# Performance work log

Hardware: AMD Instinct MI355X
Metric: run time of the kernel (lower is better)

The kernel has to match this reference:

```python
import jax, jax.numpy as jnp
import numpy as np

H = 2048          # uniform hidden size (num_in = layer_sizes[i] = num_out)
L = 8             # number of stacked LSTM cells = len(layer_sizes) + 1


def setup_inputs() -> dict:
    key = jax.random.key(0)
    ks = jax.random.split(key, 7)
    s = 1.0 / np.sqrt(H)  # torch default uniform(-1/sqrt(H), 1/sqrt(H)) scale
    return {
        "x": jax.random.normal(ks[0], (H,), dtype=jnp.float32),
        "w_ih": jax.random.normal(ks[1], (L, 4 * H, H), dtype=jnp.float32) * s,
        "w_hh": jax.random.normal(ks[2], (L, 4 * H, H), dtype=jnp.float32) * s,
        "b_ih": jax.random.normal(ks[3], (L, 4 * H), dtype=jnp.float32) * s,
        "b_hh": jax.random.normal(ks[4], (L, 4 * H), dtype=jnp.float32) * s,
        "h0": jax.random.uniform(ks[5], (L, 1, H), dtype=jnp.float32),
        "c0": jax.random.uniform(ks[6], (L, 1, H), dtype=jnp.float32),
    }


def _lstm_cell(x, h, c, w_ih, w_hh, b_ih, b_hh):
    # x, h, c: [1, H]; w_*: [4H, H]; PyTorch gate order: i, f, g, o
    gates = x @ w_ih.T + b_ih + h @ w_hh.T + b_hh  # [1, 4H]
    i, f, g, o = jnp.split(gates, 4, axis=-1)
    c_new = jax.nn.sigmoid(f) * c + jax.nn.sigmoid(i) * jnp.tanh(g)
    h_new = jax.nn.sigmoid(o) * jnp.tanh(c_new)
    return h_new, c_new


def reference(x, w_ih, w_hh, b_ih, b_hh, h0, c0):
    # seq_len = 1, batch = 1 (forward() does x.view(1, 1, -1))
    out = x.reshape(1, H)
    for l in range(L):
        h_new, _ = _lstm_cell(out, h0[l], c0[l], w_ih[l], w_hh[l], b_ih[l], b_hh[l])
        out = h_new
        if l < L - 1:  # tanh between layers, but not after the last cell
            out = jnp.tanh(out)
    return out.reshape(1, 1, H)
```

## Files before the change

kernel.cpp:

```cpp
#include <hip/hip_runtime.h>

#define HSZ 2048
#define NL  8

__global__ __launch_bounds__(256) void lstm_layer_kernel(
    const float* __restrict__ in,
    const float* __restrict__ w_ih,
    const float* __restrict__ w_hh,
    const float* __restrict__ b_ih,
    const float* __restrict__ b_hh,
    const float* __restrict__ h0,
    const float* __restrict__ c0,
    float* __restrict__ out,
    int apply_tanh)
{
    const int j    = blockIdx.x;
    const int wave = threadIdx.x >> 6;
    const int lane = threadIdx.x & 63;
    const int row  = wave * HSZ + j;

    const float4* __restrict__ wih4 = (const float4*)(w_ih + (size_t)row * HSZ);
    const float4* __restrict__ whh4 = (const float4*)(w_hh + (size_t)row * HSZ);
    const float4* __restrict__ in4  = (const float4*)in;
    const float4* __restrict__ h04  = (const float4*)h0;

    float acc = 0.f;
    #pragma unroll
    for (int it = 0; it < 8; ++it) {
        const int k = it * 64 + lane;
        float4 a  = wih4[k];
        float4 b  = whh4[k];
        float4 xv = in4[k];
        float4 hv = h04[k];
        acc += a.x * xv.x + a.y * xv.y + a.z * xv.z + a.w * xv.w;
        acc += b.x * hv.x + b.y * hv.y + b.z * hv.z + b.w * hv.w;
    }

    #pragma unroll
    for (int off = 32; off > 0; off >>= 1)
        acc += __shfl_down(acc, off, 64);

    __shared__ float gates[4];
    if (lane == 0) gates[wave] = acc + b_ih[row] + b_hh[row];
    __syncthreads();

    if (threadIdx.x == 0) {
        const float gi = gates[0];
        const float gf = gates[1];
        const float gg = gates[2];
        const float go = gates[3];
        const float si = 1.f / (1.f + __expf(-gi));
        const float sf = 1.f / (1.f + __expf(-gf));
        const float so = 1.f / (1.f + __expf(-go));
        const float tg = tanhf(gg);
        float c_new = sf * c0[j] + si * tg;
        float h     = so * tanhf(c_new);
        if (apply_tanh) h = tanhf(h);
        out[j] = h;
    }
}

extern "C" void kernel_launch(void* const* d_in, const int* in_sizes, int n_in,
                              void* d_out, int out_size, void* d_ws, size_t ws_size,
                              hipStream_t stream) {
    const float* x    = (const float*)d_in[0];
    const float* w_ih = (const float*)d_in[1];
    const float* w_hh = (const float*)d_in[2];
    const float* b_ih = (const float*)d_in[3];
    const float* b_hh = (const float*)d_in[4];
    const float* h0   = (const float*)d_in[5];
    const float* c0   = (const float*)d_in[6];
    float* out  = (float*)d_out;
    float* buf0 = (float*)d_ws;
    float* buf1 = buf0 + HSZ;

    const float* cur = x;
    for (int l = 0; l < NL; ++l) {
        float* o = (l == NL - 1) ? out : ((l & 1) ? buf1 : buf0);
        lstm_layer_kernel<<<HSZ, 256, 0, stream>>>(
            cur,
            w_ih + (size_t)l * 4 * HSZ * HSZ,
            w_hh + (size_t)l * 4 * HSZ * HSZ,
            b_ih + (size_t)l * 4 * HSZ,
            b_hh + (size_t)l * 4 * HSZ,
            h0 + (size_t)l * HSZ,
            c0 + (size_t)l * HSZ,
            o,
            (l < NL - 1) ? 1 : 0);
        cur = o;
    }
}
```

Baseline: 215.1 us.

## Fuse all LSTM layers into one persistent kernel with grid-wide atomic barrier

Replaces eight per-layer launches with a single persistent kernel of 1024 blocks, each handling two hidden units across all layers, synchronized between layers by an atomic counter barrier reset via memset. It removes launch overhead and inter-kernel gaps. It relies on all blocks being co-resident and adds spin-barrier latency plus a memset per call; the dot loops are also split into separate input and hidden passes.

After: 851.0 us. +295.7%, slower.

```diff
diff --git a/kernel.cpp b/kernel.cpp
--- a/kernel.cpp
+++ b/kernel.cpp
@@ -1,10 +1,24 @@
 #include <hip/hip_runtime.h>
 
-#define HSZ 2048
-#define NL  8
+#define HSZ  2048
+#define NL   8
+#define NBLK 1024
+#define NTHR 512
 
-__global__ __launch_bounds__(256) void lstm_layer_kernel(
-    const float* __restrict__ in,
+__device__ __forceinline__ void grid_sync(unsigned* cnt) {
+    __syncthreads();
+    if (threadIdx.x == 0) {
+        __threadfence();
+        __hip_atomic_fetch_add(cnt, 1u, __ATOMIC_RELEASE, __HIP_MEMORY_SCOPE_AGENT);
+        while (__hip_atomic_load(cnt, __ATOMIC_RELAXED, __HIP_MEMORY_SCOPE_AGENT) < NBLK)
+            __builtin_amdgcn_s_sleep(2);
+        (void)__hip_atomic_load(cnt, __ATOMIC_ACQUIRE, __HIP_MEMORY_SCOPE_AGENT);
+    }
+    __syncthreads();
+}
+
+__global__ __launch_bounds__(NTHR, 8) void lstm_fused_kernel(
+    const float* __restrict__ x,
     const float* __restrict__ w_ih,
     const float* __restrict__ w_hh,
     const float* __restrict__ b_ih,
@@ -12,51 +26,73 @@
     const float* __restrict__ h0,
     const float* __restrict__ c0,
     float* __restrict__ out,
-    int apply_tanh)
+    float* __restrict__ buf0,
+    float* __restrict__ buf1,
+    unsigned* __restrict__ bar_cnt)
 {
-    const int j    = blockIdx.x;
     const int wave = threadIdx.x >> 6;
     const int lane = threadIdx.x & 63;
-    const int row  = wave * HSZ + j;
+    const int gate = wave & 3;
+    const int j    = blockIdx.x + NBLK * (wave >> 2);
+    const int row  = gate * HSZ + j;
 
-    const float4* __restrict__ wih4 = (const float4*)(w_ih + (size_t)row * HSZ);
-    const float4* __restrict__ whh4 = (const float4*)(w_hh + (size_t)row * HSZ);
-    const float4* __restrict__ in4  = (const float4*)in;
-    const float4* __restrict__ h04  = (const float4*)h0;
+    __shared__ float gates[2][4];
 
-    float acc = 0.f;
-    #pragma unroll
-    for (int it = 0; it < 8; ++it) {
-        const int k = it * 64 + lane;
-        float4 a  = wih4[k];
-        float4 b  = whh4[k];
-        float4 xv = in4[k];
-        float4 hv = h04[k];
-        acc += a.x * xv.x + a.y * xv.y + a.z * xv.z + a.w * xv.w;
-        acc += b.x * hv.x + b.y * hv.y + b.z * hv.z + b.w * hv.w;
-    }
+    const float* cur = x;
+    for (int l = 0; l < NL; ++l) {
+        const float4* __restrict__ wih4 =
+            (const float4*)(w_ih + (size_t)l * 4 * HSZ * HSZ + (size_t)row * HSZ);
+        const float4* __restrict__ whh4 =
+            (const float4*)(w_hh + (size_t)l * 4 * HSZ * HSZ + (size_t)row * HSZ);
+        const float4* __restrict__ in4 = (const float4*)cur;
+        const float4* __restrict__ h4  = (const float4*)(h0 + (size_t)l * HSZ);
 
-    #pragma unroll
-    for (int off = 32; off > 0; off >>= 1)
-        acc += __shfl_down(acc, off, 64);
+        float acc = 0.f;
+        #pragma unroll
+        for (int it = 0; it < 8; ++it) {
+            const int k = it * 64 + lane;
+            float4 a  = wih4[k];
+            float4 xv = in4[k];
+            acc += a.x * xv.x + a.y * xv.y + a.z * xv.z + a.w * xv.w;
+        }
+        #pragma unroll
+        for (int it = 0; it < 8; ++it) {
+            const int k = it * 64 + lane;
+            float4 b  = whh4[k];
+            float4 hv = h4[k];
+            acc += b.x * hv.x + b.y * hv.y + b.z * hv.z + b.w * hv.w;
+        }
 
-    __shared__ float gates[4];
-    if (lane == 0) gates[wave] = acc + b_ih[row] + b_hh[row];
-    __syncthreads();
+        #pragma unroll
+        for (int off = 32; off > 0; off >>= 1)
+            acc += __shfl_down(acc, off, 64);
 
-    if (threadIdx.x == 0) {
-        const float gi = gates[0];
-        const float gf = gates[1];
-        const float gg = gates[2];
-        const float go = gates[3];
-        const float si = 1.f / (1.f + __expf(-gi));
-        const float sf = 1.f / (1.f + __expf(-gf));
-        const float so = 1.f / (1.f + __expf(-go));
-        const float tg = tanhf(gg);
-        float c_new = sf * c0[j] + si * tg;
-        float h     = so * tanhf(c_new);
-        if (apply_tanh) h = tanhf(h);
-        out[j] = h;
+        if (lane == 0)
+            gates[wave >> 2][gate] = acc + b_ih[(size_t)l * 4 * HSZ + row]
+                                         + b_hh[(size_t)l * 4 * HSZ + row];
+        __syncthreads();
+
+        float* obuf = (l == NL - 1) ? out : ((l & 1) ? buf1 : buf0);
+        if (threadIdx.x < 2) {
+            const int jj = blockIdx.x + (int)threadIdx.x * NBLK;
+            const float gi = gates[threadIdx.x][0];
+            const float gf = gates[threadIdx.x][1];
+            const float gg = gates[threadIdx.x][2];
+            const float go = gates[threadIdx.x][3];
+            const float si = 1.f / (1.f + __expf(-gi));
+            const float sf = 1.f / (1.f + __expf(-gf));
+            const float so = 1.f / (1.f + __expf(-go));
+            const float tg = tanhf(gg);
+            const float c_new = sf * c0[(size_t)l * HSZ + jj] + si * tg;
+            float h = so * tanhf(c_new);
+            if (l < NL - 1) h = tanhf(h);
+            obuf[jj] = h;
+        }
+
+        if (l < NL - 1) {
+            grid_sync(bar_cnt + l);
+            cur = obuf;
+        }
     }
 }
 
@@ -70,23 +106,13 @@
     const float* b_hh = (const float*)d_in[4];
     const float* h0   = (const float*)d_in[5];
     const float* c0   = (const float*)d_in[6];
-    float* out  = (float*)d_out;
-    float* buf0 = (float*)d_ws;
+    float* out = (float*)d_out;
+
+    unsigned* bar_cnt = (unsigned*)d_ws;
+    float* buf0 = (float*)((char*)d_ws + 256);
     float* buf1 = buf0 + HSZ;
 
-    const float* cur = x;
-    for (int l = 0; l < NL; ++l) {
-        float* o = (l == NL - 1) ? out : ((l & 1) ? buf1 : buf0);
-        lstm_layer_kernel<<<HSZ, 256, 0, stream>>>(
-            cur,
-            w_ih + (size_t)l * 4 * HSZ * HSZ,
-            w_hh + (size_t)l * 4 * HSZ * HSZ,
-            b_ih + (size_t)l * 4 * HSZ,
-            b_hh + (size_t)l * 4 * HSZ,
-            h0 + (size_t)l * HSZ,
-            c0 + (size_t)l * HSZ,
-            o,
-            (l < NL - 1) ? 1 : 0);
-        cur = o;
-    }
+    hipMemsetAsync(bar_cnt, 0, (NL - 1) * sizeof(unsigned), stream);
+    lstm_fused_kernel<<<NBLK, NTHR, 0, stream>>>(
+        x, w_ih, w_hh, b_ih, b_hh, h0, c0, out, buf0, buf1, bar_cnt);
 }
```

## Fuse all LSTM layers into one persistent kernel with grid-wide atomic barriers

Applied to the files above, without the earlier changes.

Replaces the eight per-layer launches with a single kernel of 2048 blocks that step through the layers, synchronising through hierarchical atomic counters (64 groups plus a master counter) held in workspace. Each block computes the recurrent w_hh·h0 dot product for the next layer before waiting on the barrier, which overlaps that weight streaming with the inter-layer dependency. Weights are read with nontemporal loads and the layer input is staged in LDS. This relies on all 2048 blocks being co-resident (8 per CU via launch bounds); otherwise the spin barrier deadlocks. It also adds a memset launch.

Measured after the change: 409.7 us. 90.5% more time.

```diff
diff --git a/kernel.cpp b/kernel.cpp
--- a/kernel.cpp
+++ b/kernel.cpp
@@ -1,10 +1,46 @@
 #include <hip/hip_runtime.h>
 
-#define HSZ 2048
-#define NL  8
+#define HSZ   2048
+#define NL    8
+#define NBLK  2048
+#define NTHR  256
+#define NGRP  64
+#define BPG   (NBLK/NGRP)
+#define BAR_U32 1040
 
-__global__ __launch_bounds__(256) void lstm_layer_kernel(
-    const float* __restrict__ in,
+typedef float f4 __attribute__((ext_vector_type(4)));
+
+__device__ __forceinline__ unsigned ld_rlx_u(const unsigned* p) {
+    return __hip_atomic_load(p, __ATOMIC_RELAXED, __HIP_MEMORY_SCOPE_AGENT);
+}
+__device__ __forceinline__ float ld_rlx_f(const float* p) {
+    return __hip_atomic_load(p, __ATOMIC_RELAXED, __HIP_MEMORY_SCOPE_AGENT);
+}
+__device__ __forceinline__ void st_rlx_f(float* p, float v) {
+    __hip_atomic_store(p, v, __ATOMIC_RELAXED, __HIP_MEMORY_SCOPE_AGENT);
+}
+__device__ __forceinline__ void arrive(unsigned* bar, int grp) {
+    unsigned o = __hip_atomic_fetch_add(&bar[grp * 16], 1u,
+                    __ATOMIC_RELAXED, __HIP_MEMORY_SCOPE_AGENT);
+    if (o == BPG - 1)
+        __hip_atomic_fetch_add(&bar[NGRP * 16], 1u,
+                    __ATOMIC_RELAXED, __HIP_MEMORY_SCOPE_AGENT);
+}
+
+__device__ __forceinline__ float dot8(const f4* __restrict__ w,
+                                      const f4* __restrict__ v, int lane) {
+    float acc = 0.f;
+    #pragma unroll
+    for (int i = 0; i < 8; ++i) {
+        f4 a = __builtin_nontemporal_load(&w[i * 64 + lane]);
+        f4 b = v[i * 64 + lane];
+        acc += a.x * b.x + a.y * b.y + a.z * b.z + a.w * b.w;
+    }
+    return acc;
+}
+
+__global__ __launch_bounds__(NTHR, 8) void lstm_fused(
+    const float* __restrict__ x,
     const float* __restrict__ w_ih,
     const float* __restrict__ w_hh,
     const float* __restrict__ b_ih,
@@ -12,51 +48,90 @@
     const float* __restrict__ h0,
     const float* __restrict__ c0,
     float* __restrict__ out,
-    int apply_tanh)
+    float* __restrict__ hA,
+    float* __restrict__ hB,
+    unsigned* __restrict__ bars)
 {
+    __shared__ float s_v[HSZ];
+    __shared__ float s_g[4];
+
+    const int tid  = threadIdx.x;
+    const int wave = tid >> 6;
+    const int lane = tid & 63;
     const int j    = blockIdx.x;
-    const int wave = threadIdx.x >> 6;
-    const int lane = threadIdx.x & 63;
     const int row  = wave * HSZ + j;
+    const int grp  = blockIdx.x & (NGRP - 1);
 
-    const float4* __restrict__ wih4 = (const float4*)(w_ih + (size_t)row * HSZ);
-    const float4* __restrict__ whh4 = (const float4*)(w_hh + (size_t)row * HSZ);
-    const float4* __restrict__ in4  = (const float4*)in;
-    const float4* __restrict__ h04  = (const float4*)h0;
-
-    float acc = 0.f;
-    #pragma unroll
-    for (int it = 0; it < 8; ++it) {
-        const int k = it * 64 + lane;
-        float4 a  = wih4[k];
-        float4 b  = whh4[k];
-        float4 xv = in4[k];
-        float4 hv = h04[k];
-        acc += a.x * xv.x + a.y * xv.y + a.z * xv.z + a.w * xv.w;
-        acc += b.x * hv.x + b.y * hv.y + b.z * hv.z + b.w * hv.w;
+    {
+        const f4* x4 = (const f4*)x;
+        f4* sv4 = (f4*)s_v;
+        sv4[tid]        = x4[tid];
+        sv4[tid + NTHR] = x4[tid + NTHR];
     }
-
-    #pragma unroll
-    for (int off = 32; off > 0; off >>= 1)
-        acc += __shfl_down(acc, off, 64);
-
-    __shared__ float gates[4];
-    if (lane == 0) gates[wave] = acc + b_ih[row] + b_hh[row];
     __syncthreads();
 
-    if (threadIdx.x == 0) {
-        const float gi = gates[0];
-        const float gf = gates[1];
-        const float gg = gates[2];
-        const float go = gates[3];
+    {
+        const float bs = b_ih[row] + b_hh[row];
+        const f4* wi4 = (const f4*)(w_ih + (size_t)row * HSZ);
+        const f4* wh4 = (const f4*)(w_hh + (size_t)row * HSZ);
+        float acc = dot8(wi4, (const f4*)s_v, lane)
+                  + dot8(wh4, (const f4*)h0, lane);
+        #pragma unroll
+        for (int off = 32; off; off >>= 1) acc += __shfl_down(acc, off, 64);
+        if (lane == 0) s_g[wave] = acc + bs;
+    }
+    __syncthreads();
+    if (tid == 0) {
+        const float gi = s_g[0], gf = s_g[1], gg = s_g[2], go = s_g[3];
         const float si = 1.f / (1.f + __expf(-gi));
         const float sf = 1.f / (1.f + __expf(-gf));
         const float so = 1.f / (1.f + __expf(-go));
-        const float tg = tanhf(gg);
-        float c_new = sf * c0[j] + si * tg;
-        float h     = so * tanhf(c_new);
-        if (apply_tanh) h = tanhf(h);
-        out[j] = h;
+        const float cn = sf * c0[j] + si * tanhf(gg);
+        st_rlx_f(&hA[j], tanhf(so * tanhf(cn)));
+    }
+    __syncthreads();
+    if (tid == 0) arrive(bars, grp);
+
+    float* const hbufs[2] = { hA, hB };
+    for (int l = 1; l < NL; ++l) {
+        const size_t wof = ((size_t)l * 4 * HSZ + row) * HSZ;
+
+        float acc2 = dot8((const f4*)(w_hh + wof),
+                          (const f4*)(h0 + (size_t)l * HSZ), lane);
+        const float bs = b_ih[(size_t)l * 4 * HSZ + row]
+                       + b_hh[(size_t)l * 4 * HSZ + row];
+
+        const unsigned* mstr = &bars[(size_t)(l - 1) * BAR_U32 + NGRP * 16];
+        if (tid == 0)
+            while (ld_rlx_u(mstr) < NGRP) __builtin_amdgcn_s_sleep(8);
+        __syncthreads();
+
+        const float* hin = hbufs[(l + 1) & 1];
+        #pragma unroll
+        for (int i = 0; i < 8; ++i)
+            s_v[i * NTHR + tid] = ld_rlx_f(&hin[i * NTHR + tid]);
+        __syncthreads();
+
+        float acc = dot8((const f4*)(w_ih + wof), (const f4*)s_v, lane) + acc2;
+        #pragma unroll
+        for (int off = 32; off; off >>= 1) acc += __shfl_down(acc, off, 64);
+        if (lane == 0) s_g[wave] = acc + bs;
+        __syncthreads();
+
+        if (tid == 0) {
+            const float gi = s_g[0], gf = s_g[1], gg = s_g[2], go = s_g[3];
+            const float si = 1.f / (1.f + __expf(-gi));
+            const float sf = 1.f / (1.f + __expf(-gf));
+            const float so = 1.f / (1.f + __expf(-go));
+            const float cn = sf * c0[(size_t)l * HSZ + j] + si * tanhf(gg);
+            const float h  = so * tanhf(cn);
+            if (l < NL - 1) st_rlx_f(&hbufs[l & 1][j], tanhf(h));
+            else            out[j] = h;
+        }
+        if (l < NL - 1) {
+            __syncthreads();
+            if (tid == 0) arrive(bars + (size_t)l * BAR_U32, grp);
+        }
     }
 }
 
@@ -70,23 +145,14 @@
     const float* b_hh = (const float*)d_in[4];
     const float* h0   = (const float*)d_in[5];
     const float* c0   = (const float*)d_in[6];
-    float* out  = (float*)d_out;
-    float* buf0 = (float*)d_ws;
-    float* buf1 = buf0 + HSZ;
+    float* out = (float*)d_out;
 
-    const float* cur = x;
-    for (int l = 0; l < NL; ++l) {
-        float* o = (l == NL - 1) ? out : ((l & 1) ? buf1 : buf0);
-        lstm_layer_kernel<<<HSZ, 256, 0, stream>>>(
-            cur,
-            w_ih + (size_t)l * 4 * HSZ * HSZ,
-            w_hh + (size_t)l * 4 * HSZ * HSZ,
-            b_ih + (size_t)l * 4 * HSZ,
-            b_hh + (size_t)l * 4 * HSZ,
-            h0 + (size_t)l * HSZ,
-            c0 + (size_t)l * HSZ,
-            o,
-            (l < NL - 1) ? 1 : 0);
-        cur = o;
-    }
+    unsigned* bars = (unsigned*)d_ws;
+    const size_t bars_bytes = (size_t)(NL - 1) * BAR_U32 * 4;
+    float* hA = (float*)((char*)d_ws + ((bars_bytes + 255) & ~(size_t)255));
+    float* hB = hA + HSZ;
+
+    (void)hipMemsetAsync(bars, 0, bars_bytes, stream);
+    lstm_fused<<<NBLK, NTHR, 0, stream>>>(
+        x, w_ih, w_hh, b_ih, b_hh, h0, c0, out, hA, hB, bars);
 }
```
